# Optimization experiments

Hardware: AMD Instinct MI355X
Metric: run time of the kernel (lower is better)

The kernel has to match this reference:

```python
import jax, jax.numpy as jnp
import numpy as np

B, C, V, K, H, W = 1, 3, 9, 8, 512, 512


def setup_inputs() -> dict:
    key = jax.random.key(0)
    k0, k1 = jax.random.split(key, 2)
    x = jax.random.normal(k0, (B, C, K, H, W), jnp.float32)          # FDL layers (spatial)
    y_views = jax.random.normal(k1, (B, C, V, H, W), jnp.float32)    # observed views (spatial)
    g = jnp.arange(3, dtype=jnp.float32) - 1.0                       # 3x3 camera grid positions
    uu, vv = jnp.meshgrid(g, g, indexing='ij')
    u = uu.reshape(-1)
    v = vv.reshape(-1)
    d = jnp.linspace(-2.0, 2.0, K).astype(jnp.float32)               # d_fdl disparities
    rho = jnp.full((1,), 0.3, jnp.float32)
    return {"x": x, "y_views": y_views, "u": u, "v": v, "d": d, "rho": rho}


def _pack_half_spectrum(Xf, x_c, y_c, n_proc):
    # [..., H, W] -> transpose to [..., W, H], center-roll so zero freq is at (x_c-1, y_c-1),
    # flatten x-major, keep the non-redundant half spectrum (first n_proc entries).
    Xt = jnp.swapaxes(Xf, -1, -2)
    Xt = jnp.roll(Xt, shift=(x_c - 1, y_c - 1), axis=(-2, -1))
    sh = Xt.shape
    return Xt.reshape(sh[:-2] + (sh[-2] * sh[-1],))[..., :n_proc]


def reference(x, y_views, u, v, d, rho):
    Bn, Cn, Kn = x.shape[0], x.shape[1], x.shape[2]
    Hn, Wn = x.shape[-2], x.shape[-1]
    rho = rho.reshape(())
    x_c = (Wn + 2) // 2                      # ceil((W+1)/2)
    y_c = (Hn + 2) // 2
    n_proc = Hn * (x_c - 1) + y_c            # half-spectrum size
    e0 = 1 - Hn % 2
    e1 = 1 - Wn % 2

    X = jnp.fft.fft2(x)                      # [B,C,K,H,W] complex64
    Y = jnp.fft.fft2(y_views)                # [B,C,V,H,W] complex64
    Xp = jnp.moveaxis(_pack_half_spectrum(X, x_c, y_c, n_proc), 2, 3) * rho   # [B,C,F,K]
    Yp = jnp.moveaxis(_pack_half_spectrum(Y, x_c, y_c, n_proc), 2, 3)         # [B,C,F,V]

    # centered angular frequency grids, flattened x-major to match packing order
    wx = (jnp.arange(Wn, dtype=jnp.float32) - (x_c - 1)) * (2.0 * np.pi / Wn)
    wy = (jnp.arange(Hn, dtype=jnp.float32) - (y_c - 1)) * (2.0 * np.pi / Hn)
    wx_f = jnp.repeat(wx, Hn)[:n_proc]       # [F]
    wy_f = jnp.tile(wy, Wn)[:n_proc]         # [F]

    # FDL data matrix A[f,v,k] = exp(i * d_k * (u_v*wx_f + v_v*wy_f))
    shift = u[None, :] * wx_f[:, None] + v[None, :] * wy_f[:, None]   # [F,V]
    A = jnp.exp(1j * shift[:, :, None] * d[None, None, :])            # [F,V,K] complex64
    Ah = jnp.conj(A)
    ATA = jnp.einsum('fvk,fvl->fkl', Ah, A)                           # [F,K,K]
    ATb = jnp.einsum('fvk,bcfv->bcfk', Ah, Yp)                        # [B,C,F,K]
    M = ATA + rho * jnp.eye(Kn, dtype=ATA.dtype)
    fdl = jnp.linalg.solve(M, (ATb + Xp)[..., None])[..., 0]          # [B,C,F,K]

    # pad redundant half with zeros, restore [B,C,K,H,W] layout
    fdl = jnp.pad(fdl, ((0, 0), (0, 0), (0, Hn * Wn - n_proc), (0, 0)))
    fdl = fdl.reshape(Bn, Cn, Wn, Hn, Kn).transpose(0, 1, 4, 3, 2)    # [B,C,K,H,W]

    # Hermitian (conjugate) symmetry reconstruction
    fdl = fdl.at[..., y_c:, x_c - 1:].set(jnp.conj(fdl[..., e0:y_c - 1, e1:x_c][..., ::-1, ::-1]))
    fdl = fdl.at[..., e0:y_c, x_c:].set(jnp.conj(fdl[..., y_c - 1:, e1:x_c - 1][..., ::-1, ::-1]))
    fdl = jnp.roll(fdl, shift=(1 - y_c, 1 - x_c), axis=(-2, -1))
    return jnp.fft.ifft2(fdl).real
```

## Files before the change

### kernel.cpp

```cpp
#include <hip/hip_runtime.h>
#include <math.h>

constexpr int N    = 512;
constexpr int LOGN = 9;
constexpr int NN   = N * N;
constexpr int CCH  = 3;
constexpr int KK   = 8;
constexpr int VV   = 9;
constexpr int FHALF = N * (N / 2) + (N / 2 + 1);
constexpr float PI_F = 3.14159265358979323846f;

__device__ __forceinline__ float2 cmulf(float2 a, float2 b) {
    return make_float2(a.x * b.x - a.y * b.y, a.x * b.y + a.y * b.x);
}
__device__ __forceinline__ float2 cadd(float2 a, float2 b) { return make_float2(a.x + b.x, a.y + b.y); }
__device__ __forceinline__ float2 csub(float2 a, float2 b) { return make_float2(a.x - b.x, a.y - b.y); }

template<int SG>
__device__ __forceinline__ float2 cmuli(float2 z) {
    return (SG < 0) ? make_float2(z.y, -z.x) : make_float2(-z.y, z.x);
}

template<int SG>
__device__ __forceinline__ void dft8(float2 x[8]) {
    const float c = 0.70710678118654752440f;
    float2 a0 = cadd(x[0], x[4]), a1 = cadd(x[1], x[5]);
    float2 a2 = cadd(x[2], x[6]), a3 = cadd(x[3], x[7]);
    float2 d0 = csub(x[0], x[4]), d1 = csub(x[1], x[5]);
    float2 d2 = csub(x[2], x[6]), d3 = csub(x[3], x[7]);
    float2 b0 = d0;
    float2 b1 = cmulf(d1, make_float2(c, (float)SG * c));
    float2 b2 = cmuli<SG>(d2);
    float2 b3 = cmulf(d3, make_float2(-c, (float)SG * c));
    float2 aa0 = cadd(a0, a2), aa1 = cadd(a1, a3);
    float2 ab0 = csub(a0, a2), ab1 = cmuli<SG>(csub(a1, a3));
    float2 ba0 = cadd(b0, b2), ba1 = cadd(b1, b3);
    float2 bb0 = csub(b0, b2), bb1 = cmuli<SG>(csub(b1, b3));
    x[0] = cadd(aa0, aa1); x[4] = csub(aa0, aa1);
    x[2] = cadd(ab0, ab1); x[6] = csub(ab0, ab1);
    x[1] = cadd(ba0, ba1); x[5] = csub(ba0, ba1);
    x[3] = cadd(bb0, bb1); x[7] = csub(bb0, bb1);
}

__device__ __forceinline__ void twiddle8(float2 v[8], float base) {
    float sn, cs;
    __sincosf(base, &sn, &cs);
    float2 w1 = make_float2(cs, sn);
    float2 wk = w1;
    v[1] = cmulf(v[1], wk);
    #pragma unroll
    for (int k = 2; k < 8; ++k) { wk = cmulf(wk, w1); v[k] = cmulf(v[k], wk); }
}

template<int SG>
__device__ __forceinline__ void wave_fft512(float2 v[8], float* sre, float* sim,
                                            int t, int stride, int off) {
    int t1 = t >> 3, t0 = t & 7;
    dft8<SG>(v);
    twiddle8(v, (float)SG * (2.0f * PI_F / 512.0f) * (float)t);
    #pragma unroll
    for (int k = 0; k < 8; ++k) {
        int a = (68 * k + 8 * t1 + t0) * stride + off;
        sre[a] = v[k].x; sim[a] = v[k].y;
    }
    #pragma unroll
    for (int n = 0; n < 8; ++n) {
        int a = (68 * t1 + 8 * n + t0) * stride + off;
        v[n] = make_float2(sre[a], sim[a]);
    }
    dft8<SG>(v);
    twiddle8(v, (float)SG * (2.0f * PI_F / 64.0f) * (float)t0);
    #pragma unroll
    for (int k = 0; k < 8; ++k) {
        int a = (68 * t0 + 8 * k + t1) * stride + off;
        sre[a] = v[k].x; sim[a] = v[k].y;
    }
    #pragma unroll
    for (int n = 0; n < 8; ++n) {
        int a = (68 * n + 8 * t0 + t1) * stride + off;
        v[n] = make_float2(sre[a], sim[a]);
    }
    dft8<SG>(v);
}

__global__ __launch_bounds__(256) void k_fft_r2c_rows_half(const float* __restrict__ in,
                                                           float2* __restrict__ out) {
    __shared__ float sre[4][544];
    __shared__ float sim[4][544];
    int w = threadIdx.x >> 6, t = threadIdx.x & 63;
    long long grow = (long long)blockIdx.x * 4 + w;
    const float* src = in + grow * N;
    float2 v[8];
    #pragma unroll
    for (int e = 0; e < 8; ++e) v[e] = make_float2(src[t + 64 * e], 0.0f);
    wave_fft512<-1>(v, sre[w], sim[w], t, 1, 0);
    float2* dst = out + grow * N;
    int kb = (t >> 3) + 8 * (t & 7);
    #pragma unroll
    for (int k0 = 4; k0 < 8; ++k0) dst[kb + 64 * k0] = v[k0];
    if (t == 0) dst[0] = v[0];
}

__global__ __launch_bounds__(256) void k_fft_r2c_rows(const float* __restrict__ in,
                                                      float2* __restrict__ out) {
    __shared__ float sre[4][544];
    __shared__ float sim[4][544];
    int w = threadIdx.x >> 6, t = threadIdx.x & 63;
    long long grow = (long long)blockIdx.x * 4 + w;
    const float* src = in + grow * N;
    float2 v[8];
    #pragma unroll
    for (int e = 0; e < 8; ++e) v[e] = make_float2(src[t + 64 * e], 0.0f);
    wave_fft512<-1>(v, sre[w], sim[w], t, 1, 0);
    float2* dst = out + grow * N;
    int kb = (t >> 3) + 8 * (t & 7);
    #pragma unroll
    for (int k0 = 0; k0 < 8; ++k0) dst[kb + 64 * k0] = v[k0];
}

template<int SG>
__global__ __launch_bounds__(256) void k_fft_pairswap(float2* __restrict__ data,
                                                      float scale, int lex, int sex) {
    __shared__ float sre[4][544];
    __shared__ float sim[4][544];
    int w = threadIdx.x >> 6, t = threadIdx.x & 63;
    int b = blockIdx.x;
    long long imgBase = (long long)(b >> 7) * NN;
    int pa = (b & 127) << 1;
    int rowg = pa + (w & 1) + ((w >> 1) << 8);
    const float2* src = data + imgBase + (long long)rowg * N;
    float2 v[8];
    #pragma unroll
    for (int e = 0; e < 8; ++e) v[e] = src[t + 64 * (e ^ lex)];
    __syncthreads();
    wave_fft512<SG>(v, sre[w], sim[w], t, 1, 0);
    float2* dst = data + imgBase + (long long)(rowg ^ 256) * N;
    int kb = (t >> 3) + 8 * (t & 7);
    #pragma unroll
    for (int k0 = 0; k0 < 8; ++k0) {
        float2 z = v[k0];
        dst[kb + 64 * (k0 ^ sex)] = make_float2(z.x * scale, z.y * scale);
    }
}

__global__ __launch_bounds__(256) void k_fft_cols_fwd(const float2* __restrict__ in,
                                                      float2* __restrict__ out) {
    __shared__ float tre[4896];
    __shared__ float tim[4896];
    int t = threadIdx.x;
    long long imgOff = (long long)blockIdx.y * NN;
    int bx = blockIdx.x;
    int x0 = bx ? (248 + (bx << 3)) : 0;
    {
        int xi2 = (t & 3) << 1;
        int yb  = t >> 2;
        const float2* img = in + imgOff;
        #pragma unroll
        for (int it = 0; it < 8; ++it) {
            int y = it * 64 + yb;
            float4 q = *(const float4*)&img[(long long)y * N + x0 + xi2];
            int a = y * 9 + xi2;
            tre[a] = q.x; tim[a] = q.y; tre[a + 1] = q.z; tim[a + 1] = q.w;
        }
    }
    __syncthreads();
    int w = t >> 6, lane = t & 63;
    int kb = (lane >> 3) + 8 * (lane & 7);
    #pragma unroll
    for (int r = 0; r < 2; ++r) {
        int cc = (w << 1) | r;
        float2 v[8];
        #pragma unroll
        for (int e = 0; e < 8; ++e) {
            int a = (lane + 64 * e) * 9 + cc;
            v[e] = make_float2(tre[a], tim[a]);
        }
        wave_fft512<-1>(v, tre, tim, lane, 9, cc);
        #pragma unroll
        for (int k0 = 0; k0 < 8; ++k0) {
            int a = (kb + 64 * k0) * 9 + cc;
            tre[a] = v[k0].x; tim[a] = v[k0].y;
        }
    }
    __syncthreads();
    {
        int xi = t >> 5, co = t & 31;
        float2* orow = out + imgOff + (long long)((x0 + xi) ^ 256) * N;
        #pragma unroll
        for (int it = 0; it < 8; ++it) {
            int b = it * 64 + co * 2;
            int y1 = b ^ 256;
            int a1 = y1 * 9 + xi, a2 = (y1 + 1) * 9 + xi;
            *(float4*)&orow[b] = make_float4(tre[a1], tim[a1], tre[a2], tim[a2]);
        }
    }
}

__device__ __forceinline__ void accum_pair(float2 bacc[KK], float tr[KK], float s,
                                           float d0, float dlt, float2 Yp, float2 Yn) {
    float2 Sp = make_float2(Yp.x + Yn.x, Yp.y + Yn.y);
    float2 Dm = make_float2(Yp.x - Yn.x, Yp.y - Yn.y);
    float sn, cs;
    __sincosf(s * d0, &sn, &cs);  float2 p = make_float2(cs, sn);
    __sincosf(s * dlt, &sn, &cs); float2 q = make_float2(cs, sn);
    float2 w = q;
    #pragma unroll
    for (int k = 0; k < KK; ++k) {
        bacc[k].x += p.x * Sp.x + p.y * Dm.y;
        bacc[k].y += p.x * Sp.y - p.y * Dm.x;
        if (k < KK - 1) {
            p = cmulf(p, q);
            tr[k + 1] += 2.0f * w.x;
            w = cmulf(w, q);
        }
    }
}

__device__ __forceinline__ void solve_point(float2 bacc[KK], float tr[KK], float rho) {
    float diag = tr[0] + rho;
    float L[36], Li[KK];
    #pragma unroll
    for (int j = 0; j < KK; ++j) {
        float acc = diag;
        #pragma unroll
        for (int t = 0; t < j; ++t) { float l = L[(j * (j - 1)) / 2 + t]; acc -= l * l; }
        float dj = sqrtf(acc);
        float inv = 1.0f / dj;
        Li[j] = inv;
        #pragma unroll
        for (int i = j + 1; i < KK; ++i) {
            float a = tr[i - j];
            #pragma unroll
            for (int t = 0; t < j; ++t)
                a -= L[(i * (i - 1)) / 2 + t] * L[(j * (j - 1)) / 2 + t];
            L[(i * (i - 1)) / 2 + j] = a * inv;
        }
    }
    #pragma unroll
    for (int i = 0; i < KK; ++i) {
        float2 a = bacc[i];
        #pragma unroll
        for (int t = 0; t < i; ++t) {
            float l = L[(i * (i - 1)) / 2 + t];
            a.x -= l * bacc[t].x;
            a.y -= l * bacc[t].y;
        }
        bacc[i] = make_float2(a.x * Li[i], a.y * Li[i]);
    }
    #pragma unroll
    for (int i = KK - 1; i >= 0; --i) {
        float2 a = bacc[i];
        #pragma unroll
        for (int t = i + 1; t < KK; ++t) {
            float l = L[(t * (t - 1)) / 2 + i];
            a.x -= l * bacc[t].x;
            a.y -= l * bacc[t].y;
        }
        bacc[i] = make_float2(a.x * Li[i], a.y * Li[i]);
    }
}

__global__ __launch_bounds__(256) void k_solve_ifft(const float2* __restrict__ Xs,
                                                    const float2* __restrict__ Ys,
                                                    float2* __restrict__ P,
                                                    const float* __restrict__ uu,
                                                    const float* __restrict__ vv,
                                                    const float* __restrict__ dd,
                                                    const float* __restrict__ rhop) {
    __shared__ float gre[KK][N];
    __shared__ float gim[KK][N];
    __shared__ float fsre[4][544];
    __shared__ float fsim[4][544];
    int a  = blockIdx.x;
    int ch = blockIdx.y;
    int t  = threadIdx.x;
    float rho = rhop[0];
    float d0 = dd[0], dlt = dd[1] - dd[0];
    const float C = 2.0f * PI_F / (float)N;
    float wxv = (float)(a - 256) * C;
    const float2* Xrow = Xs + (long long)ch * KK * NN + (long long)a * N;
    const float2* Yrow = Ys + (long long)ch * VV * NN + (long long)a * N;
    float wy0 = (float)(t - 256) * C;
    float wy1 = (float)(t)       * C;

    float2 bacc0[KK], bacc1[KK];
    float tr0[KK], tr1[KK];
    {
        const float2* Yc = Yrow + (long long)4 * NN;
        float2 yc0 = Yc[t], yc1 = Yc[t + 256];
        #pragma unroll
        for (int k = 0; k < KK; ++k) { bacc0[k] = yc0; bacc1[k] = yc1; }
        tr0[0] = tr1[0] = (float)VV;
        #pragma unroll
        for (int l = 1; l < KK; ++l) { tr0[l] = 1.0f; tr1[l] = 1.0f; }
    }
    #pragma unroll
    for (int j = 0; j < 4; ++j) {
        int vp = 5 + j, vn = 3 - j;
        float su = uu[vp], sv = vv[vp];
        const float2* Ypr = Yrow + (long long)vp * NN;
        const float2* Ynr = Yrow + (long long)vn * NN;
        float2 Yp0 = Ypr[t], Yn0 = Ynr[t];
        float2 Yp1 = Ypr[t + 256], Yn1 = Ynr[t + 256];
        accum_pair(bacc0, tr0, su * wxv + sv * wy0, d0, dlt, Yp0, Yn0);
        accum_pair(bacc1, tr1, su * wxv + sv * wy1, d0, dlt, Yp1, Yn1);
    }
    #pragma unroll
    for (int k = 0; k < KK; ++k) {
        const float2* Xr = Xrow + (long long)k * NN;
        float2 x0v = Xr[t], x1v = Xr[t + 256];
        bacc0[k].x += rho * x0v.x; bacc0[k].y += rho * x0v.y;
        bacc1[k].x += rho * x1v.x; bacc1[k].y += rho * x1v.y;
    }
    solve_point(bacc0, tr0, rho);
    solve_point(bacc1, tr1, rho);
    #pragma unroll
    for (int k = 0; k < KK; ++k) {
        gre[k][t] = bacc0[k].x;       gim[k][t] = bacc0[k].y;
        gre[k][t + 256] = bacc1[k].x; gim[k][t + 256] = bacc1[k].y;
    }
    __syncthreads();
    if (a == 256 && t >= 1) {
        int b = t + 256, bs = 256 - t;
        #pragma unroll
        for (int k = 0; k < KK; ++k) {
            gre[k][b] = gre[k][bs];
            gim[k][b] = -gim[k][bs];
        }
    }
    __syncthreads();

    int w = t >> 6, lane = t & 63;
    int kb = (lane >> 3) + 8 * (lane & 7);
    float sgn = ((lane >> 3) & 1) ? -1.0f : 1.0f;
    const float inv512 = 1.0f / 512.0f;
    #pragma unroll
    for (int r = 0; r < 2; ++r) {
        int k = (w << 1) | r;
        float2 v[8];
        #pragma unroll
        for (int e = 0; e < 8; ++e) {
            int idx = (lane + 64 * e) ^ 256;
            v[e] = make_float2(gre[k][idx], gim[k][idx]);
        }
        wave_fft512<1>(v, fsre[w], fsim[w], lane, 1, 0);
        float s0x = gre[k][0], s0y = gim[k][0];
        float2* Pimg = P + (long long)(ch * KK + k) * NN;
        if (a >= 1 && a <= 255) {
            float2* pmain = Pimg + (long long)(a + 256) * N;
            float2* pmirr = Pimg + (long long)(256 - a) * N;
            #pragma unroll
            for (int k0 = 0; k0 < 8; ++k0) {
                int pos = kb + 64 * k0;
                float2 W = v[k0];
                pmain[pos] = make_float2(W.x * inv512, W.y * inv512);
                pmirr[pos] = make_float2((W.x - s0x * sgn) * inv512,
                                         (-W.y + s0y * sgn) * inv512);
            }
        } else {
            float2* pmain = Pimg + (long long)(a == 0 ? 256 : 0) * N;
            #pragma unroll
            for (int k0 = 0; k0 < 8; ++k0) {
                int pos = kb + 64 * k0;
                float2 W = v[k0];
                pmain[pos] = make_float2(W.x * inv512, W.y * inv512);
            }
        }
    }
}

__global__ __launch_bounds__(256) void k_fft_cols_inv_real(const float2* __restrict__ in,
                                                           float* __restrict__ out,
                                                           float scale) {
    __shared__ float tre[4896];
    __shared__ float tim[4896];
    int t = threadIdx.x;
    long long imgOff = (long long)blockIdx.y * NN;
    int b0 = blockIdx.x << 3;
    {
        int xi2 = (t & 3) << 1;
        int yb  = t >> 2;
        const float2* img = in + imgOff;
        #pragma unroll
        for (int it = 0; it < 8; ++it) {
            int c = it * 64 + yb;
            float4 q = *(const float4*)&img[(long long)c * N + b0 + xi2];
            int a = c * 9 + xi2;
            tre[a] = q.x; tim[a] = q.y; tre[a + 1] = q.z; tim[a + 1] = q.w;
        }
    }
    __syncthreads();
    int w = t >> 6, lane = t & 63;
    int kb = (lane >> 3) + 8 * (lane & 7);
    #pragma unroll
    for (int r = 0; r < 2; ++r) {
        int cc = (w << 1) | r;
        float2 v[8];
        #pragma unroll
        for (int e = 0; e < 8; ++e) {
            int a = (lane + 64 * e) * 9 + cc;
            v[e] = make_float2(tre[a], tim[a]);
        }
        wave_fft512<1>(v, tre, tim, lane, 9, cc);
        #pragma unroll
        for (int k0 = 0; k0 < 8; ++k0)
            tre[(kb + 64 * k0) * 9 + cc] = v[k0].x;
    }
    __syncthreads();
    {
        int xi = t >> 5, co = t & 31;
        float* orow = out + (long long)blockIdx.y * NN + (long long)(b0 + xi) * N;
        #pragma unroll
        for (int it = 0; it < 4; ++it) {
            int ww = it * 128 + co * 4;
            *(float4*)&orow[ww] = make_float4(tre[ww * 9 + xi] * scale,
                                              tre[(ww + 1) * 9 + xi] * scale,
                                              tre[(ww + 2) * 9 + xi] * scale,
                                              tre[(ww + 3) * 9 + xi] * scale);
        }
    }
}

__global__ __launch_bounds__(256) void k_transpose_inplace(float2* __restrict__ data) {
    int ti = blockIdx.x, tj = blockIdx.y;
    if (ti > tj) return;
    float2* img = data + (long long)blockIdx.z * NN;
    __shared__ float2 ta[32][33];
    __shared__ float2 tb[32][33];
    int tx = threadIdx.x, ty = threadIdx.y;
    int r0 = ti << 5, c0 = tj << 5;
    bool diag = (ti == tj);
    #pragma unroll
    for (int kk = 0; kk < 4; ++kk) {
        int r = ty + (kk << 3);
        ta[r][tx] = img[(long long)(r0 + r) * N + (c0 + tx)];
        if (!diag) tb[r][tx] = img[(long long)(c0 + r) * N + (r0 + tx)];
    }
    __syncthreads();
    #pragma unroll
    for (int kk = 0; kk < 4; ++kk) {
        int r = ty + (kk << 3);
        img[(long long)(c0 + r) * N + (r0 + tx)] = ta[tx][r];
        if (!diag) img[(long long)(r0 + r) * N + (c0 + tx)] = tb[tx][r];
    }
}

__global__ __launch_bounds__(256) void k_fft_c2r_rows(const float2* __restrict__ in,
                                                      float* __restrict__ out, float scale) {
    __shared__ float sre[4][544];
    __shared__ float sim[4][544];
    int w = threadIdx.x >> 6, t = threadIdx.x & 63;
    long long grow = (long long)blockIdx.x * 4 + w;
    const float2* src = in + grow * N;
    float2 v[8];
    #pragma unroll
    for (int e = 0; e < 8; ++e) v[e] = src[t + 64 * e];
    wave_fft512<1>(v, sre[w], sim[w], t, 1, 0);
    float* dst = out + grow * N;
    int kb = (t >> 3) + 8 * (t & 7);
    #pragma unroll
    for (int k0 = 0; k0 < 8; ++k0) dst[kb + 64 * k0] = v[k0].x * scale;
}

__global__ __launch_bounds__(256) void k_solve(float2* __restrict__ Xs,
                                               const float2* __restrict__ Ys,
                                               const float* __restrict__ uu,
                                               const float* __restrict__ vv,
                                               const float* __restrict__ dd,
                                               const float* __restrict__ rhop) {
    int f = blockIdx.x * 256 + threadIdx.x;
    if (f >= FHALF) return;
    long long coffX = (long long)blockIdx.y * KK * NN;
    long long coffY = (long long)blockIdx.y * VV * NN;
    float rho = rhop[0];
    int x = f >> LOGN;
    int y = f & (N - 1);
    float wxv = (float)(x - N / 2) * (2.0f * PI_F / (float)N);
    float wyv = (float)(y - N / 2) * (2.0f * PI_F / (float)N);
    float d0 = dd[0], dlt = dd[1] - dd[0];
    float2 bacc[KK];
    float tr[KK];
    {
        float2 Yc = Ys[coffY + (long long)4 * NN + f];
        #pragma unroll
        for (int k = 0; k < KK; ++k) bacc[k] = Yc;
        tr[0] = (float)VV;
        #pragma unroll
        for (int l = 1; l < KK; ++l) tr[l] = 1.0f;
    }
    #pragma unroll
    for (int j = 0; j < 4; ++j) {
        int vp = 5 + j, vn = 3 - j;
        float s = uu[vp] * wxv + vv[vp] * wyv;
        accum_pair(bacc, tr, s, d0, dlt,
                   Ys[coffY + (long long)vp * NN + f],
                   Ys[coffY + (long long)vn * NN + f]);
    }
    #pragma unroll
    for (int k = 0; k < KK; ++k) {
        float2 Xk = Xs[coffX + (long long)k * NN + f];
        bacc[k].x += rho * Xk.x;
        bacc[k].y += rho * Xk.y;
    }
    solve_point(bacc, tr, rho);
    int xm = (N - x) & (N - 1);
    int ym = (N - y) & (N - 1);
    long long fm = (long long)xm * N + ym;
    bool conjMirror = false, zeroMirror = false;
    if (x >= 1 && x <= N / 2 - 1) {
        if (y == 0) zeroMirror = true; else conjMirror = true;
    } else if (x == N / 2 && y >= 1 && y <= N / 2 - 1) {
        conjMirror = true;
    }
    #pragma unroll
    for (int k = 0; k < KK; ++k) {
        float2* base = Xs + coffX + (long long)k * NN;
        float2 z = bacc[k];
        base[f] = z;
        if (conjMirror)      base[fm] = make_float2(z.x, -z.y);
        else if (zeroMirror) base[fm] = make_float2(0.f, 0.f);
    }
}

extern "C" void kernel_launch(void* const* d_in, const int* in_sizes, int n_in,
                              void* d_out, int out_size, void* d_ws, size_t ws_size,
                              hipStream_t stream) {
    (void)in_sizes; (void)n_in; (void)out_size;
    const float* x   = (const float*)d_in[0];
    const float* yv  = (const float*)d_in[1];
    const float* uu  = (const float*)d_in[2];
    const float* vvp = (const float*)d_in[3];
    const float* dd  = (const float*)d_in[4];
    const float* rho = (const float*)d_in[5];
    float* out = (float*)d_out;
    float2* ws = (float2*)d_ws;

    const size_t needBatchedNew = (size_t)CCH * (KK + VV + VV) * NN * sizeof(float2);
    const size_t needChanNew    = (size_t)(KK + VV + VV) * NN * sizeof(float2);
    const float invN = 1.0f / (float)N;

    if (ws_size >= needChanNew) {
        bool batched = ws_size >= needBatchedNew;
        int iters = batched ? 1 : CCH;
        int ncs   = batched ? CCH : 1;
        int nx = ncs * KK, ny = ncs * VV;
        for (int it = 0; it < iters; ++it) {
            float2* Xt = ws;
            float2* Yt = ws + (size_t)nx * NN;
            float2* Rt = Yt + (size_t)ny * NN;
            const float* xin = x  + (size_t)it * KK * NN;
            const float* yin = yv + (size_t)it * VV * NN;
            float* oout = out + (size_t)it * KK * NN;
            k_fft_r2c_rows_half<<<nx * (N / 4), 256, 0, stream>>>(xin, Rt);
            k_fft_cols_fwd<<<dim3(33, nx), 256, 0, stream>>>(Rt, Xt);
            k_fft_r2c_rows_half<<<ny * (N / 4), 256, 0, stream>>>(yin, Rt);
            k_fft_cols_fwd<<<dim3(33, ny), 256, 0, stream>>>(Rt, Yt);
            k_solve_ifft<<<dim3(257, ncs), 256, 0, stream>>>(Xt, Yt, Rt, uu, vvp, dd, rho);
            k_fft_cols_inv_real<<<dim3(N / 8, nx), 256, 0, stream>>>(Rt, oout, invN);
        }
    } else {
        for (int it = 0; it < CCH; ++it) {
            float2* Xb = ws;
            float2* Yb = ws + (size_t)KK * NN;
            const float* xin = x  + (size_t)it * KK * NN;
            const float* yin = yv + (size_t)it * VV * NN;
            float* oout = out + (size_t)it * KK * NN;
            k_fft_r2c_rows<<<KK * (N / 4), 256, 0, stream>>>(xin, Xb);
            k_fft_r2c_rows<<<VV * (N / 4), 256, 0, stream>>>(yin, Yb);
            k_transpose_inplace<<<dim3(16, 16, KK), dim3(32, 8), 0, stream>>>(Xb);
            k_transpose_inplace<<<dim3(16, 16, VV), dim3(32, 8), 0, stream>>>(Yb);
            k_fft_pairswap<-1><<<KK * (N / 4), 256, 0, stream>>>(Xb, 1.0f, 0, 4);
            k_fft_pairswap<-1><<<VV * (N / 4), 256, 0, stream>>>(Yb, 1.0f, 0, 4);
            k_solve<<<dim3((FHALF + 255) / 256, 1), 256, 0, stream>>>(Xb, Yb, uu, vvp, dd, rho);
            k_fft_pairswap<1><<<KK * (N / 4), 256, 0, stream>>>(Xb, invN, 4, 0);
            k_transpose_inplace<<<dim3(16, 16, KK), dim3(32, 8), 0, stream>>>(Xb);
            k_fft_c2r_rows<<<KK * (N / 4), 256, 0, stream>>>(Xb, oout, invN);
        }
    }
}
```

Before: 188.0 us.

## Pack two real rows per complex FFT and merge X/Y forward passes

The forward row FFT now packs two real input rows into one complex 512-point transform and separates the two half spectra through a shared-memory mirror lookup. This halves the row-FFT arithmetic and wave count. The X and Y images are also handled in one row launch and one column launch instead of two each, which cuts kernel launches. The workspace requirement grows because Rt now needs room for all X and Y rows, so the batched path needs a larger buffer. The extra LDS pass adds some shared-memory traffic.

```diff
diff --git a/kernel.cpp b/kernel.cpp
--- a/kernel.cpp
+++ b/kernel.cpp
@@ -83,22 +83,44 @@
     dft8<SG>(v);
 }
 
-__global__ __launch_bounds__(256) void k_fft_r2c_rows_half(const float* __restrict__ in,
+__global__ __launch_bounds__(256) void k_fft_r2c_rows_pack(const float* __restrict__ inx,
+                                                           const float* __restrict__ iny,
+                                                           int nximg,
                                                            float2* __restrict__ out) {
     __shared__ float sre[4][544];
     __shared__ float sim[4][544];
     int w = threadIdx.x >> 6, t = threadIdx.x & 63;
-    long long grow = (long long)blockIdx.x * 4 + w;
-    const float* src = in + grow * N;
+    long long gp = (long long)blockIdx.x * 4 + w;
+    long long row0 = gp * 2;
+    long long xrows = (long long)nximg * N;
+    const float* src0 = (row0 < xrows) ? (inx + row0 * N)
+                                       : (iny + (row0 - xrows) * N);
+    const float* src1 = src0 + N;
     float2 v[8];
     #pragma unroll
-    for (int e = 0; e < 8; ++e) v[e] = make_float2(src[t + 64 * e], 0.0f);
+    for (int e = 0; e < 8; ++e) v[e] = make_float2(src0[t + 64 * e], src1[t + 64 * e]);
     wave_fft512<-1>(v, sre[w], sim[w], t, 1, 0);
-    float2* dst = out + grow * N;
     int kb = (t >> 3) + 8 * (t & 7);
     #pragma unroll
-    for (int k0 = 4; k0 < 8; ++k0) dst[kb + 64 * k0] = v[k0];
-    if (t == 0) dst[0] = v[0];
+    for (int k0 = 0; k0 < 8; ++k0) {
+        int p = kb + 64 * k0;
+        sre[w][p] = v[k0].x; sim[w][p] = v[k0].y;
+    }
+    float2* dst0 = out + row0 * N;
+    float2* dst1 = dst0 + N;
+    #pragma unroll
+    for (int k0 = 4; k0 < 8; ++k0) {
+        int p  = kb + 64 * k0;
+        int mp = 512 - p;
+        float zmx = sre[w][mp], zmy = sim[w][mp];
+        float2 Zp = v[k0];
+        dst0[p] = make_float2(0.5f * (Zp.x + zmx), 0.5f * (Zp.y - zmy));
+        dst1[p] = make_float2(0.5f * (Zp.y + zmy), 0.5f * (zmx - Zp.x));
+    }
+    if (t == 0) {
+        dst0[0] = make_float2(v[0].x, 0.0f);
+        dst1[0] = make_float2(v[0].y, 0.0f);
+    }
 }
 
 __global__ __launch_bounds__(256) void k_fft_r2c_rows(const float* __restrict__ in,
@@ -535,26 +557,24 @@
     float* out = (float*)d_out;
     float2* ws = (float2*)d_ws;
 
-    const size_t needBatchedNew = (size_t)CCH * (KK + VV + VV) * NN * sizeof(float2);
-    const size_t needChanNew    = (size_t)(KK + VV + VV) * NN * sizeof(float2);
+    const size_t needBatchedPack = (size_t)2 * CCH * (KK + VV) * NN * sizeof(float2);
+    const size_t needChanPack    = (size_t)2 * (KK + VV) * NN * sizeof(float2);
     const float invN = 1.0f / (float)N;
 
-    if (ws_size >= needChanNew) {
-        bool batched = ws_size >= needBatchedNew;
+    if (ws_size >= needChanPack) {
+        bool batched = ws_size >= needBatchedPack;
         int iters = batched ? 1 : CCH;
         int ncs   = batched ? CCH : 1;
         int nx = ncs * KK, ny = ncs * VV;
         for (int it = 0; it < iters; ++it) {
             float2* Xt = ws;
             float2* Yt = ws + (size_t)nx * NN;
-            float2* Rt = Yt + (size_t)ny * NN;
+            float2* Rt = ws + (size_t)(nx + ny) * NN;
             const float* xin = x  + (size_t)it * KK * NN;
             const float* yin = yv + (size_t)it * VV * NN;
             float* oout = out + (size_t)it * KK * NN;
-            k_fft_r2c_rows_half<<<nx * (N / 4), 256, 0, stream>>>(xin, Rt);
-            k_fft_cols_fwd<<<dim3(33, nx), 256, 0, stream>>>(Rt, Xt);
-            k_fft_r2c_rows_half<<<ny * (N / 4), 256, 0, stream>>>(yin, Rt);
-            k_fft_cols_fwd<<<dim3(33, ny), 256, 0, stream>>>(Rt, Yt);
+            k_fft_r2c_rows_pack<<<(nx + ny) * (N / 8), 256, 0, stream>>>(xin, yin, nx, Rt);
+            k_fft_cols_fwd<<<dim3(33, nx + ny), 256, 0, stream>>>(Rt, Xt);
             k_solve_ifft<<<dim3(257, ncs), 256, 0, stream>>>(Xt, Yt, Rt, uu, vvp, dd, rho);
             k_fft_cols_inv_real<<<dim3(N / 8, nx), 256, 0, stream>>>(Rt, oout, invN);
         }
```

Result: faster. 179.5 us (-4.5%).
